# Optimization experiments

Hardware: AMD Instinct MI355X
Metric: run time of the kernel (lower is better)

## Reference

```python
import jax, jax.numpy as jnp
import numpy as np


def setup_inputs() -> dict:
    key = jax.random.key(0)
    k1, k2, k3 = jax.random.split(key, 3)
    B, S, Q, K, D = 64, 512, 800, 4, 64
    q_data = jax.random.normal(k1, (B, S, Q), dtype=jnp.float32)
    r_data = jax.random.randint(k2, (B, S), 0, K)
    # learned params (xavier-ish scale)
    Wq = jax.random.normal(k3, (D, Q), dtype=jnp.float32) * (0.5 * (2.0 / (Q + D)) ** 0.5)
    bq = jnp.zeros((D,), dtype=jnp.float32)
    Wr = jax.random.normal(jax.random.fold_in(key, 7), (1, K), dtype=jnp.float32) * (0.5 * (2.0 / (K + 1)) ** 0.5)
    br = jnp.zeros((1,), dtype=jnp.float32)
    return {"q_data": q_data, "r_data": r_data, "Wq": Wq, "bq": bq,
            "Wr": Wr, "br": br, "n_questions": Q, "n_cats": K}


def reference(q_data, r_data, Wq, bq, Wr, br, n_questions, n_cats):
    # Vectorized over (batch, seq): original looped over t in python.
    K = n_cats
    k_idx = jnp.arange(K, dtype=q_data.dtype)                      # [K]
    dist = jnp.abs(k_idx[None, None, :] - r_data[..., None].astype(q_data.dtype)) / (K - 1)  # [B,S,K]
    weights = jnp.maximum(1.0 - dist, 0.0)                        # [B,S,K]
    # response_weights: Linear(K -> 1) then sigmoid -> scalar gate per (b,s)
    gate = jax.nn.sigmoid(jnp.einsum('bsk,ok->bso', weights, Wr) + br)  # [B,S,1]
    weighted_q = q_data * gate                                    # [B,S,Q]
    # question_embed: Linear(Q -> D)
    out = jnp.einsum('bsq,dq->bsd', weighted_q, Wq) + bq          # [B,S,D]
    return out
```

## Files before the change

kernel.cpp:

```cpp
#include <hip/hip_runtime.h>
#include <hip/hip_bf16.h>


#define QD 800
#define DD 64
#define M_TOTAL 32768
#define KT 25

typedef __attribute__((ext_vector_type(8))) short bf16x8;
typedef __attribute__((ext_vector_type(4))) float f32x4;

static __device__ __forceinline__ short f2bf(float f) {
  union { __hip_bfloat16 h; short s; } u;
  u.h = __float2bfloat16(f);
  return u.s;
}

static __device__ __forceinline__ bf16x8 load_split8(const float* __restrict__ p) {
  f32x4 lo = *reinterpret_cast<const f32x4*>(p);
  f32x4 hi = *reinterpret_cast<const f32x4*>(p + 16);
  bf16x8 r;
  r[0] = f2bf(lo.x); r[1] = f2bf(lo.y); r[2] = f2bf(lo.z); r[3] = f2bf(lo.w);
  r[4] = f2bf(hi.x); r[5] = f2bf(hi.y); r[6] = f2bf(hi.z); r[7] = f2bf(hi.w);
  return r;
}

__global__ void convert_wq_kernel(const float* __restrict__ Wq, short* __restrict__ Bb) {
  int idx = blockIdx.x * 256 + threadIdx.x;
  int kt = idx >> 8;
  int acc = (idx >> 6) & 3;
  int lane = idx & 63;
  int l15 = lane & 15, lhi = lane >> 4;
  const float* p = Wq + (acc * 16 + l15) * QD + kt * 32 + lhi * 4;
  bf16x8 r = load_split8(p);
  *reinterpret_cast<bf16x8*>(Bb + (size_t)idx * 8) = r;
}

template <bool USE_WS>
__global__ __launch_bounds__(256, 2) void sold_kernel(
    const float* __restrict__ q, const int* __restrict__ rdat,
    const short* __restrict__ Bb, const float* __restrict__ Wq,
    const float* __restrict__ bq, const float* __restrict__ Wr,
    const float* __restrict__ br, float* __restrict__ out) {
  const int lane = threadIdx.x & 63;
  const int wave = threadIdx.x >> 6;
  const int l15 = lane & 15;
  const int lhi = lane >> 4;
  const int m0 = blockIdx.x * 64 + wave * 16;

  const float* aptr = q + (size_t)(m0 + l15) * QD + lhi * 4;
  const short* bptr = Bb + (size_t)lane * 8;
  const float* w0 = Wq + (0 * 16 + l15) * QD + lhi * 4;
  const float* w1 = Wq + (1 * 16 + l15) * QD + lhi * 4;
  const float* w2 = Wq + (2 * 16 + l15) * QD + lhi * 4;
  const float* w3 = Wq + (3 * 16 + l15) * QD + lhi * 4;

  f32x4 acc0 = {0.f, 0.f, 0.f, 0.f};
  f32x4 acc1 = {0.f, 0.f, 0.f, 0.f};
  f32x4 acc2 = {0.f, 0.f, 0.f, 0.f};
  f32x4 acc3 = {0.f, 0.f, 0.f, 0.f};

#pragma unroll 5
  for (int kt = 0; kt < KT; ++kt) {
    bf16x8 a = load_split8(aptr + kt * 32);
    bf16x8 b0, b1, b2, b3;
    if constexpr (USE_WS) {
      const short* bp = bptr + kt * 2048;
      b0 = *reinterpret_cast<const bf16x8*>(bp + 0 * 512);
      b1 = *reinterpret_cast<const bf16x8*>(bp + 1 * 512);
      b2 = *reinterpret_cast<const bf16x8*>(bp + 2 * 512);
      b3 = *reinterpret_cast<const bf16x8*>(bp + 3 * 512);
    } else {
      b0 = load_split8(w0 + kt * 32);
      b1 = load_split8(w1 + kt * 32);
      b2 = load_split8(w2 + kt * 32);
      b3 = load_split8(w3 + kt * 32);
    }
    acc0 = __builtin_amdgcn_mfma_f32_16x16x32_bf16(a, b0, acc0, 0, 0, 0);
    acc1 = __builtin_amdgcn_mfma_f32_16x16x32_bf16(a, b1, acc1, 0, 0, 0);
    acc2 = __builtin_amdgcn_mfma_f32_16x16x32_bf16(a, b2, acc2, 0, 0, 0);
    acc3 = __builtin_amdgcn_mfma_f32_16x16x32_bf16(a, b3, acc3, 0, 0, 0);
  }

  float wr[4] = {Wr[0], Wr[1], Wr[2], Wr[3]};
  float brv = br[0];
  float lut[4];
  const float inv3 = 1.0f / 3.0f;
#pragma unroll
  for (int r = 0; r < 4; ++r) {
    float s = brv;
#pragma unroll
    for (int k = 0; k < 4; ++k) {
      float w = fmaxf(1.0f - fabsf((float)(k - r)) * inv3, 0.0f);
      s += w * wr[k];
    }
    lut[r] = 1.0f / (1.0f + __expf(-s));
  }

  float bqv0 = bq[0 * 16 + l15];
  float bqv1 = bq[1 * 16 + l15];
  float bqv2 = bq[2 * 16 + l15];
  float bqv3 = bq[3 * 16 + l15];

#pragma unroll
  for (int r = 0; r < 4; ++r) {
    int row = m0 + lhi * 4 + r;
    float g = lut[rdat[row]];
    float* orow = out + (size_t)row * DD + l15;
    orow[0]  = acc0[r] * g + bqv0;
    orow[16] = acc1[r] * g + bqv1;
    orow[32] = acc2[r] * g + bqv2;
    orow[48] = acc3[r] * g + bqv3;
  }
}

extern "C" void kernel_launch(void* const* d_in, const int* in_sizes, int n_in,
                              void* d_out, int out_size, void* d_ws, size_t ws_size,
                              hipStream_t stream) {
  const float* q    = (const float*)d_in[0];
  const int*   rdat = (const int*)d_in[1];
  const float* Wq   = (const float*)d_in[2];
  const float* bq   = (const float*)d_in[3];
  const float* Wr   = (const float*)d_in[4];
  const float* br   = (const float*)d_in[5];
  float* out = (float*)d_out;

  const size_t need_ws = (size_t)KT * 4 * 64 * 8 * sizeof(short);
  if (ws_size >= need_ws) {
    short* Bb = (short*)d_ws;
    convert_wq_kernel<<<KT, 256, 0, stream>>>(Wq, Bb);
    sold_kernel<true><<<M_TOTAL / 64, 256, 0, stream>>>(q, rdat, Bb, Wq, bq, Wr, br, out);
  } else {
    sold_kernel<false><<<M_TOTAL / 64, 256, 0, stream>>>(q, rdat, nullptr, Wq, bq, Wr, br, out);
  }
}
```

Baseline: 179.8 us.

## Split K across wave pairs and reduce partial sums through shared memory

Each block now covers 32 rows instead of 64, and pairs of waves split the 25-step K loop (13 and 12 steps) over the same 16-row tile. The partial accumulators are combined through an LDS buffer after a block barrier. The grid doubles, the launch bounds go up to 4 blocks per SM, and the K loops are fully unrolled. The aim is more parallelism and more memory requests in flight on this memory-bound GEMM, at the cost of an LDS round trip, a barrier, and extra B-matrix reads per row.

```diff
diff --git a/kernel.cpp b/kernel.cpp
--- a/kernel.cpp
+++ b/kernel.cpp
@@ -6,6 +6,7 @@
 #define DD 64
 #define M_TOTAL 32768
 #define KT 25
+#define KSPLIT 13
 
 typedef __attribute__((ext_vector_type(8))) short bf16x8;
 typedef __attribute__((ext_vector_type(4))) float f32x4;
@@ -16,13 +17,16 @@
   return u.s;
 }
 
-static __device__ __forceinline__ bf16x8 load_split8(const float* __restrict__ p) {
-  f32x4 lo = *reinterpret_cast<const f32x4*>(p);
-  f32x4 hi = *reinterpret_cast<const f32x4*>(p + 16);
+static __device__ __forceinline__ bf16x8 pack8(f32x4 lo, f32x4 hi) {
   bf16x8 r;
   r[0] = f2bf(lo.x); r[1] = f2bf(lo.y); r[2] = f2bf(lo.z); r[3] = f2bf(lo.w);
   r[4] = f2bf(hi.x); r[5] = f2bf(hi.y); r[6] = f2bf(hi.z); r[7] = f2bf(hi.w);
   return r;
+}
+
+static __device__ __forceinline__ bf16x8 load_split8(const float* __restrict__ p) {
+  return pack8(*reinterpret_cast<const f32x4*>(p),
+               *reinterpret_cast<const f32x4*>(p + 16));
 }
 
 __global__ void convert_wq_kernel(const float* __restrict__ Wq, short* __restrict__ Bb) {
@@ -36,8 +40,37 @@
   *reinterpret_cast<bf16x8*>(Bb + (size_t)idx * 8) = r;
 }
 
+template <int CNT, bool USE_WS>
+static __device__ __forceinline__ void kloop(
+    const float* __restrict__ ap, const short* __restrict__ bp,
+    const float* __restrict__ w0, const float* __restrict__ w1,
+    const float* __restrict__ w2, const float* __restrict__ w3,
+    f32x4& acc0, f32x4& acc1, f32x4& acc2, f32x4& acc3) {
+#pragma unroll
+  for (int i = 0; i < CNT; ++i) {
+    bf16x8 a = load_split8(ap + i * 32);
+    bf16x8 b0, b1, b2, b3;
+    if constexpr (USE_WS) {
+      const short* p = bp + i * 2048;
+      b0 = *reinterpret_cast<const bf16x8*>(p + 0 * 512);
+      b1 = *reinterpret_cast<const bf16x8*>(p + 1 * 512);
+      b2 = *reinterpret_cast<const bf16x8*>(p + 2 * 512);
+      b3 = *reinterpret_cast<const bf16x8*>(p + 3 * 512);
+    } else {
+      b0 = load_split8(w0 + i * 32);
+      b1 = load_split8(w1 + i * 32);
+      b2 = load_split8(w2 + i * 32);
+      b3 = load_split8(w3 + i * 32);
+    }
+    acc0 = __builtin_amdgcn_mfma_f32_16x16x32_bf16(a, b0, acc0, 0, 0, 0);
+    acc1 = __builtin_amdgcn_mfma_f32_16x16x32_bf16(a, b1, acc1, 0, 0, 0);
+    acc2 = __builtin_amdgcn_mfma_f32_16x16x32_bf16(a, b2, acc2, 0, 0, 0);
+    acc3 = __builtin_amdgcn_mfma_f32_16x16x32_bf16(a, b3, acc3, 0, 0, 0);
+  }
+}
+
 template <bool USE_WS>
-__global__ __launch_bounds__(256, 2) void sold_kernel(
+__global__ __launch_bounds__(256, 4) void sold_kernel(
     const float* __restrict__ q, const int* __restrict__ rdat,
     const short* __restrict__ Bb, const float* __restrict__ Wq,
     const float* __restrict__ bq, const float* __restrict__ Wr,
@@ -46,40 +79,48 @@
   const int wave = threadIdx.x >> 6;
   const int l15 = lane & 15;
   const int lhi = lane >> 4;
-  const int m0 = blockIdx.x * 64 + wave * 16;
+  const int tile = wave & 1;
+  const int khalf = wave >> 1;
+  const int m0 = blockIdx.x * 32 + tile * 16;
+  const int kt0 = khalf ? KSPLIT : 0;
 
-  const float* aptr = q + (size_t)(m0 + l15) * QD + lhi * 4;
-  const short* bptr = Bb + (size_t)lane * 8;
-  const float* w0 = Wq + (0 * 16 + l15) * QD + lhi * 4;
-  const float* w1 = Wq + (1 * 16 + l15) * QD + lhi * 4;
-  const float* w2 = Wq + (2 * 16 + l15) * QD + lhi * 4;
-  const float* w3 = Wq + (3 * 16 + l15) * QD + lhi * 4;
+  const float* ap = q + (size_t)(m0 + l15) * QD + kt0 * 32 + lhi * 4;
+  const short* bp = Bb + (size_t)kt0 * 2048 + lane * 8;
+  const float* w0 = Wq + (0 * 16 + l15) * QD + kt0 * 32 + lhi * 4;
+  const float* w1 = Wq + (1 * 16 + l15) * QD + kt0 * 32 + lhi * 4;
+  const float* w2 = Wq + (2 * 16 + l15) * QD + kt0 * 32 + lhi * 4;
+  const float* w3 = Wq + (3 * 16 + l15) * QD + kt0 * 32 + lhi * 4;
 
   f32x4 acc0 = {0.f, 0.f, 0.f, 0.f};
   f32x4 acc1 = {0.f, 0.f, 0.f, 0.f};
   f32x4 acc2 = {0.f, 0.f, 0.f, 0.f};
   f32x4 acc3 = {0.f, 0.f, 0.f, 0.f};
 
-#pragma unroll 5
-  for (int kt = 0; kt < KT; ++kt) {
-    bf16x8 a = load_split8(aptr + kt * 32);
-    bf16x8 b0, b1, b2, b3;
-    if constexpr (USE_WS) {
-      const short* bp = bptr + kt * 2048;
-      b0 = *reinterpret_cast<const bf16x8*>(bp + 0 * 512);
-      b1 = *reinterpret_cast<const bf16x8*>(bp + 1 * 512);
-      b2 = *reinterpret_cast<const bf16x8*>(bp + 2 * 512);
-      b3 = *reinterpret_cast<const bf16x8*>(bp + 3 * 512);
-    } else {
-      b0 = load_split8(w0 + kt * 32);
-      b1 = load_split8(w1 + kt * 32);
-      b2 = load_split8(w2 + kt * 32);
-      b3 = load_split8(w3 + kt * 32);
+  if (khalf == 0) {
+    kloop<KSPLIT, USE_WS>(ap, bp, w0, w1, w2, w3, acc0, acc1, acc2, acc3);
+  } else {
+    kloop<KT - KSPLIT, USE_WS>(ap, bp, w0, w1, w2, w3, acc0, acc1, acc2, acc3);
+  }
+
+  __shared__ float comb[2][16][64];
+  if (khalf == 1) {
+#pragma unroll
+    for (int r = 0; r < 4; ++r) {
+      comb[tile][0 * 4 + r][lane] = acc0[r];
+      comb[tile][1 * 4 + r][lane] = acc1[r];
+      comb[tile][2 * 4 + r][lane] = acc2[r];
+      comb[tile][3 * 4 + r][lane] = acc3[r];
     }
-    acc0 = __builtin_amdgcn_mfma_f32_16x16x32_bf16(a, b0, acc0, 0, 0, 0);
-    acc1 = __builtin_amdgcn_mfma_f32_16x16x32_bf16(a, b1, acc1, 0, 0, 0);
-    acc2 = __builtin_amdgcn_mfma_f32_16x16x32_bf16(a, b2, acc2, 0, 0, 0);
-    acc3 = __builtin_amdgcn_mfma_f32_16x16x32_bf16(a, b3, acc3, 0, 0, 0);
+  }
+  __syncthreads();
+  if (khalf == 1) return;
+
+#pragma unroll
+  for (int r = 0; r < 4; ++r) {
+    acc0[r] += comb[tile][0 * 4 + r][lane];
+    acc1[r] += comb[tile][1 * 4 + r][lane];
+    acc2[r] += comb[tile][2 * 4 + r][lane];
+    acc3[r] += comb[tile][3 * 4 + r][lane];
   }
 
   float wr[4] = {Wr[0], Wr[1], Wr[2], Wr[3]};
@@ -126,11 +167,12 @@
   float* out = (float*)d_out;
 
   const size_t need_ws = (size_t)KT * 4 * 64 * 8 * sizeof(short);
+  const int grid = M_TOTAL / 32;
   if (ws_size >= need_ws) {
     short* Bb = (short*)d_ws;
     convert_wq_kernel<<<KT, 256, 0, stream>>>(Wq, Bb);
-    sold_kernel<true><<<M_TOTAL / 64, 256, 0, stream>>>(q, rdat, Bb, Wq, bq, Wr, br, out);
+    sold_kernel<true><<<grid, 256, 0, stream>>>(q, rdat, Bb, Wq, bq, Wr, br, out);
   } else {
-    sold_kernel<false><<<M_TOTAL / 64, 256, 0, stream>>>(q, rdat, nullptr, Wq, bq, Wr, br, out);
+    sold_kernel<false><<<grid, 256, 0, stream>>>(q, rdat, nullptr, Wq, bq, Wr, br, out);
   }
 }
```

Measured after the change: 177.1 us. Within noise of the previous version (-1.5%).
